# Kernel optimization log

Measured on AMD Instinct MI355X. Metric: run time of the kernel, lower is better.

## Reference

```python
import jax, jax.numpy as jnp
import numpy as np

NUM_HEADS = 8
SPLIT = 2  # split_size; idx=0 -> H_sp=H, W_sp=SPLIT (horizontal stripes)


def setup_inputs() -> dict:
    key = jax.random.key(0)
    k1, k2, k3 = jax.random.split(key, 3)
    B, C, H, W = 4, 64, 128, 128
    temp = jax.random.normal(k1, (B, 3, C, H, W), dtype=jnp.float32)
    conv_w = jax.random.normal(k2, (C, 1, 3, 3), dtype=jnp.float32) * 0.1  # depthwise OIHW
    conv_b = jax.random.normal(k3, (C,), dtype=jnp.float32) * 0.1
    return {"temp": temp, "conv_w": conv_w, "conv_b": conv_b}


def reference(temp, conv_w, conv_b):
    B, _, C, H, W = temp.shape
    hd = C // NUM_HEADS
    scale = hd ** (-0.5)
    H_sp, W_sp = H, SPLIT  # idx == 0

    # symmetric pad to multiples of window size (faithful to original; zero here)
    H_pad = (H_sp - H % H_sp) % H_sp
    W_pad = (W_sp - W % W_sp) % W_sp
    top, left = H_pad // 2, W_pad // 2
    x = jnp.pad(temp, ((0, 0), (0, 0), (0, 0), (top, H_pad - top), (left, W_pad - left)))
    H_, W_ = H + H_pad, W + W_pad
    q, k, v = x[:, 0], x[:, 1], x[:, 2]  # each [B,C,H_,W_]

    nW = (H_ // H_sp) * (W_ // W_sp)
    N = H_sp * W_sp  # tokens per window

    def im2cswin(t):
        # [B,C,H_,W_] -> [B*nW, heads, N, hd]
        w = t.reshape(B, C, H_ // H_sp, H_sp, W_ // W_sp, W_sp)
        w = w.transpose(0, 2, 4, 3, 5, 1).reshape(-1, N, C)
        return w.reshape(-1, N, NUM_HEADS, hd).transpose(0, 2, 1, 3)

    qh = im2cswin(q) * scale
    kh = im2cswin(k)

    # v windows as images [B*nW, C, H_sp, W_sp] for depthwise LePE conv
    vw = v.reshape(B, C, H_ // H_sp, H_sp, W_ // W_sp, W_sp)
    vw = vw.transpose(0, 2, 4, 1, 3, 5).reshape(-1, C, H_sp, W_sp)
    rpe = jax.lax.conv_general_dilated(
        vw, conv_w, window_strides=(1, 1), padding='SAME',
        feature_group_count=C, dimension_numbers=('NCHW', 'OIHW', 'NCHW'))
    rpe = rpe + conv_b[None, :, None, None]

    vh = vw.reshape(-1, NUM_HEADS, hd, N).transpose(0, 1, 3, 2)    # [B*nW,h,N,hd]
    rpeh = rpe.reshape(-1, NUM_HEADS, hd, N).transpose(0, 1, 3, 2)

    attn = jax.nn.softmax(jnp.einsum('whnd,whmd->whnm', qh, kh), axis=-1)
    out = jnp.einsum('whnm,whmd->whnd', attn, vh) + rpeh           # [B*nW,h,N,hd]

    out = out.transpose(0, 2, 1, 3).reshape(-1, N, C)              # [B*nW,N,C]
    # windows2img + crop
    out = out.reshape(B, H_ // H_sp, W_ // W_sp, H_sp, W_sp, C)
    out = out.transpose(0, 1, 3, 2, 4, 5).reshape(B, H_, W_, C)
    out = out[:, top:H + top, left:W + left, :]
    return out.reshape(B, H * W, C)
```

## Files before the change

### kernel.cpp

```cpp
#include <hip/hip_runtime.h>
#include <hip/hip_bf16.h>
#include <stdint.h>


typedef __attribute__((ext_vector_type(8))) short bf16x8;
typedef __attribute__((ext_vector_type(4))) short bf16x4;
typedef __attribute__((ext_vector_type(4))) float f32x4;

static __device__ __forceinline__ uint32_t pk2(float x, float y) {
    union { __hip_bfloat162 h2; uint32_t u; } c;
    c.h2 = __float22bfloat162_rn(make_float2(x, y));
    return c.u;
}
static __device__ __forceinline__ float bflo(uint32_t u){ return __uint_as_float(u<<16); }
static __device__ __forceinline__ float bfhi(uint32_t u){ return __uint_as_float(u & 0xffff0000u); }

static __device__ __forceinline__ f32x4 mfma16x16x16bf16(bf16x4 a, bf16x4 b, f32x4 c) {
#if __has_builtin(__builtin_amdgcn_mfma_f32_16x16x16bf16_1k)
    return __builtin_amdgcn_mfma_f32_16x16x16bf16_1k(a, b, c, 0, 0, 0);
#else
    f32x4 d;
    asm volatile("v_mfma_f32_16x16x16_bf16 %0, %1, %2, %3\n\ts_nop 7\n\ts_nop 7"
                 : "=v"(d) : "v"(a), "v"(b), "v"(c));
    return d;
#endif
}

__global__ __launch_bounds__(512, 4)
void lepe_attn(const float* __restrict__ temp,
               const float* __restrict__ conv_w,
               const float* __restrict__ conv_b,
               float* __restrict__ out)
{
    __shared__ __align__(16) char smem[55328];
    char* q_s = smem;
    char* k_s = smem + 18432;
    char* v_t = smem + 36864;
    float* cw_s = (float*)(smem + 54016);

    const int tid  = threadIdx.x;
    const int wave = tid >> 6, lane = tid & 63;
    const int lr = lane & 15, quad = lane >> 4;
    const int head  = wave & 3;
    const int qbase = (wave >> 2) * 8;

    const int bid = blockIdx.x;
    const int x  = bid & 7;
    int t_ = bid >> 3;
    const int hf = t_ & 1;  t_ >>= 1;
    const int wj = t_ & 7;
    const int b  = t_ >> 3;
    const int wi = x * 8 + wj;
    const int c0 = hf * 32;

    const size_t cstr = 16384, sstr = 64 * cstr;
    const float qs = 0.35355339059327373f * 1.4426950408889634f;

    {
        const int cg = tid & 31, hh0 = tid >> 5;
        const float* qp = temp + (size_t)b*3*sstr + (size_t)(c0+cg)*cstr + wi*2;
        #pragma unroll
        for (int i = 0; i < 8; ++i) {
            int h = i*16 + hh0;
            float2 fq = *(const float2*)(qp + (size_t)h*128);
            uint32_t uq = pk2(fq.x*qs, fq.y*qs);
            *(uint16_t*)(q_s + (2*h)*72   + cg*2) = (uint16_t)uq;
            *(uint16_t*)(q_s + (2*h+1)*72 + cg*2) = (uint16_t)(uq>>16);
            float2 fk = *(const float2*)(qp + sstr + (size_t)h*128);
            uint32_t uk = pk2(fk.x, fk.y);
            *(uint16_t*)(k_s + (2*h)*72   + cg*2) = (uint16_t)uk;
            *(uint16_t*)(k_s + (2*h+1)*72 + cg*2) = (uint16_t)(uk>>16);
            float2 fv = *(const float2*)(qp + 2*sstr + (size_t)h*128);
            *(uint32_t*)(v_t + cg*536 + 4*h + 4) = pk2(fv.x, fv.y);
        }
        for (int j = tid; j < 288; j += 512) cw_s[j] = conv_w[c0*9 + j];
        if (tid < 32) {
            *(uint32_t*)(v_t + tid*536)       = 0;
            *(uint32_t*)(v_t + tid*536 + 516) = 0;
            cw_s[288 + tid] = conv_b[c0 + tid];
        }
    }
    __syncthreads();

    const f32x4 zf = {0.f, 0.f, 0.f, 0.f};
    const uint2 z2 = make_uint2(0, 0);
    uint2 kf[16]; uint2 vf[16];
    #pragma unroll
    for (int T = 0; T < 16; ++T) {
        uint2 kk = *(const uint2*)(k_s + (T*16 + lr)*72 + head*16 + (quad & 1)*8);
        kf[T] = (quad < 2) ? kk : z2;
        uint2 vv = *(const uint2*)(v_t + (head*8 + (lane&7))*536 + 4 + (T*16 + quad*4)*2);
        vf[T] = (lr < 8) ? vv : z2;
    }
    __syncthreads();

    {
        const int ch = tid & 31, seg = tid >> 5;
        const char* base = v_t + ch*536 + seg*32;
        uint32_t d[10];
        *(uint4*)(d+0) = *(const uint4*)(base);
        *(uint4*)(d+4) = *(const uint4*)(base+16);
        *(uint2*)(d+8) = *(const uint2*)(base+32);
        float w9[9];
        #pragma unroll
        for (int k = 0; k < 9; ++k) w9[k] = cw_s[ch*9 + k];
        const float bia = cw_s[288 + ch];
        #pragma unroll
        for (int tt = 0; tt < 16; ++tt) {
            int tok = seg*16 + tt;
            int w01 = tok & 1;
            int L = (tt >> 1) * 2;
            float rp = bia;
            #pragma unroll
            for (int dy = 0; dy < 3; ++dy) {
                #pragma unroll
                for (int wp = 0; wp < 2; ++wp) {
                    int idx = L + 2*dy + wp;
                    uint32_t dw = d[idx >> 1];
                    float tap = (idx & 1) ? bfhi(dw) : bflo(dw);
                    rp = fmaf(w9[dy*3 + wp + 1 - w01], tap, rp);
                }
            }
            union { __hip_bfloat16 h; uint16_t u; } cv;
            cv.h = __float2bfloat16(rp);
            *(uint16_t*)(k_s + tok*72 + ch*2) = cv.u;
        }
    }
    __syncthreads();

    #pragma unroll 1
    for (int qg0 = 0; qg0 < 8; ++qg0) {
        const int qg = qbase + qg0;
        uint2 qq = *(const uint2*)(q_s + (qg*16 + lr)*72 + head*16 + (quad & 1)*8);
        union { uint2 u; bf16x4 h4; } qf; qf.u = (quad < 2) ? qq : z2;
        f32x4 acc = zf;
        float rsum = 0.f;
        #pragma unroll
        for (int T = 0; T < 16; ++T) {
            union { uint2 u; bf16x4 h4; } kfu; kfu.u = kf[T];
            f32x4 sc = mfma16x16x16bf16(kfu.h4, qf.h4, zf);
            float e0 = __builtin_amdgcn_exp2f(sc[0]);
            float e1 = __builtin_amdgcn_exp2f(sc[1]);
            float e2 = __builtin_amdgcn_exp2f(sc[2]);
            float e3 = __builtin_amdgcn_exp2f(sc[3]);
            rsum += (e0 + e1) + (e2 + e3);
            union { uint2 u; bf16x4 h4; } pb; pb.u = make_uint2(pk2(e0,e1), pk2(e2,e3));
            union { uint2 u; bf16x4 h4; } vfu; vfu.u = vf[T];
            acc = mfma16x16x16bf16(vfu.h4, pb.h4, acc);
        }
        float rs = rsum;
        rs += __shfl_xor(rs, 16);
        rs += __shfl_xor(rs, 32);
        const float rinv = __builtin_amdgcn_rcpf(rs);
        if (quad < 2) {
            int tok = qg*16 + lr;
            int h = tok >> 1, w01 = tok & 1;
            uint2 rp2 = *(const uint2*)(k_s + tok*72 + (head*8 + quad*4)*2);
            float4 ov;
            ov.x = fmaf(acc[0], rinv, bflo(rp2.x));
            ov.y = fmaf(acc[1], rinv, bfhi(rp2.x));
            ov.z = fmaf(acc[2], rinv, bflo(rp2.y));
            ov.w = fmaf(acc[3], rinv, bfhi(rp2.y));
            size_t addr = (size_t)b*1048576 + (size_t)(h*128 + wi*2 + w01)*64
                        + c0 + head*8 + quad*4;
            *(float4*)(out + addr) = ov;
        }
    }
}

extern "C" void kernel_launch(void* const* d_in, const int* in_sizes, int n_in,
                              void* d_out, int out_size, void* d_ws, size_t ws_size,
                              hipStream_t stream) {
    const float* temp = (const float*)d_in[0];
    const float* cw   = (const float*)d_in[1];
    const float* cb   = (const float*)d_in[2];
    float* o = (float*)d_out;
    (void)in_sizes; (void)n_in; (void)out_size; (void)d_ws; (void)ws_size;
    lepe_attn<<<dim3(512), dim3(512), 0, stream>>>(temp, cw, cb, o);
}
```

Before: 130.1 us.

## Remap blocks to one head across four windows with compact shared layout

```diff
diff --git a/kernel.cpp b/kernel.cpp
--- a/kernel.cpp
+++ b/kernel.cpp
@@ -3,7 +3,6 @@
 #include <stdint.h>
 
 
-typedef __attribute__((ext_vector_type(8))) short bf16x8;
 typedef __attribute__((ext_vector_type(4))) short bf16x4;
 typedef __attribute__((ext_vector_type(4))) float f32x4;
 
@@ -14,6 +13,13 @@
 }
 static __device__ __forceinline__ float bflo(uint32_t u){ return __uint_as_float(u<<16); }
 static __device__ __forceinline__ float bfhi(uint32_t u){ return __uint_as_float(u & 0xffff0000u); }
+
+static __device__ __forceinline__ uint2 ld2(const char* p) {
+    uint2 r;
+    r.x = *(const uint32_t*)(p);
+    r.y = *(const uint32_t*)(p + 4);
+    return r;
+}
 
 static __device__ __forceinline__ f32x4 mfma16x16x16bf16(bf16x4 a, bf16x4 b, f32x4 c) {
 #if __has_builtin(__builtin_amdgcn_mfma_f32_16x16x16bf16_1k)
@@ -26,58 +32,73 @@
 #endif
 }
 
+#define QK_TOK_STR 20
+#define QK_WIN_STR 5120
+#define V_CH_STR   536
+#define V_WIN_STR  4288
+
 __global__ __launch_bounds__(512, 4)
 void lepe_attn(const float* __restrict__ temp,
                const float* __restrict__ conv_w,
                const float* __restrict__ conv_b,
                float* __restrict__ out)
 {
-    __shared__ __align__(16) char smem[55328];
+    __shared__ __align__(16) char smem[58432];
     char* q_s = smem;
-    char* k_s = smem + 18432;
-    char* v_t = smem + 36864;
-    float* cw_s = (float*)(smem + 54016);
+    char* k_s = smem + 20480;
+    char* v_t = smem + 40960;
+    float* cw_s = (float*)(smem + 58112);
 
     const int tid  = threadIdx.x;
     const int wave = tid >> 6, lane = tid & 63;
     const int lr = lane & 15, quad = lane >> 4;
-    const int head  = wave & 3;
+    const int win   = wave & 3;
     const int qbase = (wave >> 2) * 8;
 
     const int bid = blockIdx.x;
     const int x  = bid & 7;
     int t_ = bid >> 3;
-    const int hf = t_ & 1;  t_ >>= 1;
-    const int wj = t_ & 7;
-    const int b  = t_ >> 3;
-    const int wi = x * 8 + wj;
-    const int c0 = hf * 32;
+    const int wjh  = t_ & 1;  t_ >>= 1;
+    const int head = t_ & 7;
+    const int b    = t_ >> 3;
+    const int wi   = x*8 + wjh*4 + win;
 
     const size_t cstr = 16384, sstr = 64 * cstr;
     const float qs = 0.35355339059327373f * 1.4426950408889634f;
 
     {
-        const int cg = tid & 31, hh0 = tid >> 5;
-        const float* qp = temp + (size_t)b*3*sstr + (size_t)(c0+cg)*cstr + wi*2;
-        #pragma unroll
-        for (int i = 0; i < 8; ++i) {
-            int h = i*16 + hh0;
-            float2 fq = *(const float2*)(qp + (size_t)h*128);
-            uint32_t uq = pk2(fq.x*qs, fq.y*qs);
-            *(uint16_t*)(q_s + (2*h)*72   + cg*2) = (uint16_t)uq;
-            *(uint16_t*)(q_s + (2*h+1)*72 + cg*2) = (uint16_t)(uq>>16);
-            float2 fk = *(const float2*)(qp + sstr + (size_t)h*128);
-            uint32_t uk = pk2(fk.x, fk.y);
-            *(uint16_t*)(k_s + (2*h)*72   + cg*2) = (uint16_t)uk;
-            *(uint16_t*)(k_s + (2*h+1)*72 + cg*2) = (uint16_t)(uk>>16);
-            float2 fv = *(const float2*)(qp + 2*sstr + (size_t)h*128);
-            *(uint32_t*)(v_t + cg*536 + 4*h + 4) = pk2(fv.x, fv.y);
-        }
-        for (int j = tid; j < 288; j += 512) cw_s[j] = conv_w[c0*9 + j];
+        const int cg = wave;
+        const int hg = lane >> 1, hf1 = lane & 1;
+        const int w0 = hf1 * 2;
+        const float* bp = temp + (size_t)b*3*sstr + (size_t)(head*8 + cg)*cstr
+                        + x*16 + wjh*8 + hf1*4;
+        #pragma unroll
+        for (int i = 0; i < 4; ++i) {
+            int h = i*32 + hg;
+            float4 fq = *(const float4*)(bp + (size_t)h*128);
+            uint32_t a0 = pk2(fq.x*qs, fq.y*qs);
+            uint32_t a1 = pk2(fq.z*qs, fq.w*qs);
+            *(uint16_t*)(q_s + w0*QK_WIN_STR     + (2*h)*QK_TOK_STR   + cg*2) = (uint16_t)a0;
+            *(uint16_t*)(q_s + w0*QK_WIN_STR     + (2*h+1)*QK_TOK_STR + cg*2) = (uint16_t)(a0>>16);
+            *(uint16_t*)(q_s + (w0+1)*QK_WIN_STR + (2*h)*QK_TOK_STR   + cg*2) = (uint16_t)a1;
+            *(uint16_t*)(q_s + (w0+1)*QK_WIN_STR + (2*h+1)*QK_TOK_STR + cg*2) = (uint16_t)(a1>>16);
+            float4 fk = *(const float4*)(bp + sstr + (size_t)h*128);
+            uint32_t b0 = pk2(fk.x, fk.y);
+            uint32_t b1 = pk2(fk.z, fk.w);
+            *(uint16_t*)(k_s + w0*QK_WIN_STR     + (2*h)*QK_TOK_STR   + cg*2) = (uint16_t)b0;
+            *(uint16_t*)(k_s + w0*QK_WIN_STR     + (2*h+1)*QK_TOK_STR + cg*2) = (uint16_t)(b0>>16);
+            *(uint16_t*)(k_s + (w0+1)*QK_WIN_STR + (2*h)*QK_TOK_STR   + cg*2) = (uint16_t)b1;
+            *(uint16_t*)(k_s + (w0+1)*QK_WIN_STR + (2*h+1)*QK_TOK_STR + cg*2) = (uint16_t)(b1>>16);
+            float4 fv = *(const float4*)(bp + 2*sstr + (size_t)h*128);
+            *(uint32_t*)(v_t + w0*V_WIN_STR     + cg*V_CH_STR + 4*h + 4) = pk2(fv.x, fv.y);
+            *(uint32_t*)(v_t + (w0+1)*V_WIN_STR + cg*V_CH_STR + 4*h + 4) = pk2(fv.z, fv.w);
+        }
+        if (tid < 72) cw_s[tid] = conv_w[head*72 + tid];
+        if (tid < 8)  cw_s[72 + tid] = conv_b[head*8 + tid];
         if (tid < 32) {
-            *(uint32_t*)(v_t + tid*536)       = 0;
-            *(uint32_t*)(v_t + tid*536 + 516) = 0;
-            cw_s[288 + tid] = conv_b[c0 + tid];
+            int vw = tid >> 3, vc = tid & 7;
+            *(uint32_t*)(v_t + vw*V_WIN_STR + vc*V_CH_STR)       = 0;
+            *(uint32_t*)(v_t + vw*V_WIN_STR + vc*V_CH_STR + 516) = 0;
         }
     }
     __syncthreads();
@@ -87,24 +108,28 @@
     uint2 kf[16]; uint2 vf[16];
     #pragma unroll
     for (int T = 0; T < 16; ++T) {
-        uint2 kk = *(const uint2*)(k_s + (T*16 + lr)*72 + head*16 + (quad & 1)*8);
+        uint2 kk = ld2(k_s + win*QK_WIN_STR + (T*16 + lr)*QK_TOK_STR + (quad & 1)*8);
         kf[T] = (quad < 2) ? kk : z2;
-        uint2 vv = *(const uint2*)(v_t + (head*8 + (lane&7))*536 + 4 + (T*16 + quad*4)*2);
+        uint2 vv = ld2(v_t + win*V_WIN_STR + (lane & 7)*V_CH_STR + 4 + (T*16 + quad*4)*2);
         vf[T] = (lr < 8) ? vv : z2;
     }
     __syncthreads();
 
     {
-        const int ch = tid & 31, seg = tid >> 5;
-        const char* base = v_t + ch*536 + seg*32;
+        const int w2  = tid >> 7;
+        const int chl = (tid >> 4) & 7;
+        const int seg = tid & 15;
+        const char* base = v_t + w2*V_WIN_STR + chl*V_CH_STR + seg*32;
         uint32_t d[10];
-        *(uint4*)(d+0) = *(const uint4*)(base);
-        *(uint4*)(d+4) = *(const uint4*)(base+16);
+        *(uint2*)(d+0) = *(const uint2*)(base);
+        *(uint2*)(d+2) = *(const uint2*)(base+8);
+        *(uint2*)(d+4) = *(const uint2*)(base+16);
+        *(uint2*)(d+6) = *(const uint2*)(base+24);
         *(uint2*)(d+8) = *(const uint2*)(base+32);
         float w9[9];
         #pragma unroll
-        for (int k = 0; k < 9; ++k) w9[k] = cw_s[ch*9 + k];
-        const float bia = cw_s[288 + ch];
+        for (int k = 0; k < 9; ++k) w9[k] = cw_s[chl*9 + k];
+        const float bia = cw_s[72 + chl];
         #pragma unroll
         for (int tt = 0; tt < 16; ++tt) {
             int tok = seg*16 + tt;
@@ -123,7 +148,7 @@
             }
             union { __hip_bfloat16 h; uint16_t u; } cv;
             cv.h = __float2bfloat16(rp);
-            *(uint16_t*)(k_s + tok*72 + ch*2) = cv.u;
+            *(uint16_t*)(k_s + w2*QK_WIN_STR + tok*QK_TOK_STR + chl*2) = cv.u;
         }
     }
     __syncthreads();
@@ -131,7 +156,7 @@
     #pragma unroll 1
     for (int qg0 = 0; qg0 < 8; ++qg0) {
         const int qg = qbase + qg0;
-        uint2 qq = *(const uint2*)(q_s + (qg*16 + lr)*72 + head*16 + (quad & 1)*8);
+        uint2 qq = ld2(q_s + win*QK_WIN_STR + (qg*16 + lr)*QK_TOK_STR + (quad & 1)*8);
         union { uint2 u; bf16x4 h4; } qf; qf.u = (quad < 2) ? qq : z2;
         f32x4 acc = zf;
         float rsum = 0.f;
@@ -155,14 +180,14 @@
         if (quad < 2) {
             int tok = qg*16 + lr;
             int h = tok >> 1, w01 = tok & 1;
-            uint2 rp2 = *(const uint2*)(k_s + tok*72 + (head*8 + quad*4)*2);
+            uint2 rp2 = ld2(k_s + win*QK_WIN_STR + tok*QK_TOK_STR + quad*8);
             float4 ov;
             ov.x = fmaf(acc[0], rinv, bflo(rp2.x));
             ov.y = fmaf(acc[1], rinv, bfhi(rp2.x));
             ov.z = fmaf(acc[2], rinv, bflo(rp2.y));
             ov.w = fmaf(acc[3], rinv, bfhi(rp2.y));
             size_t addr = (size_t)b*1048576 + (size_t)(h*128 + wi*2 + w01)*64
-                        + c0 + head*8 + quad*4;
+                        + head*8 + quad*4;
             *(float4*)(out + addr) = ov;
         }
     }
```

New measurement: 115.4 us. 1.13x faster.
